# Kernel tuning notes

Hardware: AMD Instinct MI355X
Metric: run time of the kernel (lower is better)

Reference implementation:

```python
import jax, jax.numpy as jnp
import numpy as np
from jax import lax

B, CIN, H, W = 64, 3, 64, 64
HID = 128          # hidden_dim == embedding_dim
K = 1024           # num_embeddings
BETA = 0.25        # commitment cost


def _conv(x, w, b, stride):
    # torch Conv2d, padding=0, NCHW / OIHW weights
    y = lax.conv_general_dilated(x, w, (stride, stride), 'VALID',
                                 dimension_numbers=('NCHW', 'OIHW', 'NCHW'))
    return y + b[None, :, None, None]


def _conv_transpose(x, w, b, stride):
    # torch ConvTranspose2d, padding=0; w is [Cin, Cout, kh, kw] (torch layout)
    kh, kw = w.shape[2], w.shape[3]
    w2 = jnp.flip(w, (2, 3)).transpose(1, 0, 2, 3)  # -> OIHW, spatially flipped
    y = lax.conv_general_dilated(x, w2, (1, 1),
                                 [(kh - 1, kh - 1), (kw - 1, kw - 1)],
                                 lhs_dilation=(stride, stride),
                                 dimension_numbers=('NCHW', 'OIHW', 'NCHW'))
    return y + b[None, :, None, None]


def setup_inputs() -> dict:
    key = jax.random.key(0)
    ks = jax.random.split(key, 10)
    s = 0.05
    return {
        'x':      jax.random.normal(ks[0], (B, CIN, H, W), jnp.float32),
        'enc_w1': jax.random.normal(ks[1], (HID, CIN, 4, 4), jnp.float32) * s,
        'enc_b1': jnp.zeros((HID,), jnp.float32),
        'enc_w2': jax.random.normal(ks[2], (HID, HID, 2, 2), jnp.float32) * s,
        'enc_b2': jnp.zeros((HID,), jnp.float32),
        'codebook': jax.random.uniform(ks[3], (K, HID), jnp.float32,
                                       minval=-1.0 / K, maxval=1.0 / K),
        'dec_w1': jax.random.normal(ks[4], (HID, HID, 2, 2), jnp.float32) * s,
        'dec_b1': jnp.zeros((HID,), jnp.float32),
        'dec_w2': jax.random.normal(ks[5], (HID, CIN, 4, 4), jnp.float32) * s,
        'dec_b2': jnp.zeros((CIN,), jnp.float32),
    }


def reference(x, enc_w1, enc_b1, enc_w2, enc_b2, codebook,
              dec_w1, dec_b1, dec_w2, dec_b2):
    # ---- encoder ----
    z = jax.nn.relu(_conv(x, enc_w1, enc_b1, 2))
    z = jax.nn.relu(_conv(z, enc_w2, enc_b2, 1))   # [B, HID, 30, 30]

    # ---- vector quantizer (faithful to torch reshape semantics) ----
    D = HID
    flat = z.reshape(-1, D)                        # [N, D], C-order rows
    # squared euclidean distances (argmin identical to torch.cdist argmin)
    d2 = (jnp.sum(flat * flat, axis=1, keepdims=True)
          - 2.0 * flat @ codebook.T
          + jnp.sum(codebook * codebook, axis=1)[None, :])  # [N, K]
    idx = jnp.argmin(d2, axis=1)                   # [N]
    quantized = codebook[idx].reshape(z.shape)

    e_latent = jnp.mean((lax.stop_gradient(quantized) - z) ** 2)
    q_latent = jnp.mean((quantized - lax.stop_gradient(z)) ** 2)
    loss = q_latent + BETA * e_latent

    q_st = z + lax.stop_gradient(quantized - z)    # straight-through

    n = flat.shape[0]
    avg_probs = jnp.zeros((K,), z.dtype).at[idx].add(1.0) / n
    perplexity = jnp.exp(-jnp.sum(avg_probs * jnp.log(avg_probs + 1e-10)))

    # ---- decoder ----
    y = jax.nn.relu(_conv_transpose(q_st, dec_w1, dec_b1, 1))
    x_recon = _conv_transpose(y, dec_w2, dec_b2, 2)  # [B, 3, 64, 64]
    return x_recon, loss, perplexity
```

## Files before the change

kernel.cpp:

```cpp
#include <hip/hip_runtime.h>

#define B_    64
#define CIN_  3
#define HW_   64
#define HID_  128
#define K_    1024
#define H1_   31
#define H2_   30
#define NROWS_ 57600
#define NELEM_ 7372800

typedef __bf16 bf16_t;
typedef __attribute__((ext_vector_type(8))) __bf16 bf16x8;
typedef __attribute__((ext_vector_type(4))) float f32x4;
typedef __attribute__((ext_vector_type(16))) float f32x16;

__global__ __launch_bounds__(256) void wprep_k(const float* __restrict__ ew1,
    const float* __restrict__ ew2, const float* __restrict__ dw1,
    const float* __restrict__ dw2, const float* __restrict__ cb,
    bf16_t* __restrict__ wc1, bf16_t* __restrict__ wc2,
    bf16_t* __restrict__ wd1, bf16_t* __restrict__ wt2,
    bf16_t* __restrict__ cbb, float* __restrict__ cnorm,
    unsigned* __restrict__ hist, float* __restrict__ sse) {
  int id = blockIdx.x * 256 + threadIdx.x;
  int t = id >> 14, co = (id >> 7) & 127, ci = id & 127;
  wc2[id] = (bf16_t)ew2[(co * 128 + ci) * 4 + t];
  wd1[id] = (bf16_t)dw1[(ci * 128 + co) * 4 + (3 - t)];
  if (id < 8192) {
    int n = id >> 9, k = id & 511;
    int tap = k >> 7, c = k & 127;
    if (n < 12) {
      int nco = n >> 2, ph = (n >> 1) & 1, pw = n & 1;
      int off = (tap >> 1) * 8 + (tap & 1) * 2;
      wt2[id] = (bf16_t)dw2[c * 48 + nco * 16 + ph * 4 + pw + off];
    } else {
      wt2[id] = (bf16_t)0.f;
    }
    int c1 = id >> 6, k1 = id & 63;
    wc1[id] = (bf16_t)(k1 < 48 ? ew1[c1 * 48 + k1] : 0.f);
  }
  if (id < K_) {
    float s0 = 0.f;
    for (int d = 0; d < HID_; d += 4) {
      float4 v = *(const float4*)&cb[id * HID_ + d];
      bf16_t tt[4] = {(bf16_t)v.x, (bf16_t)v.y, (bf16_t)v.z, (bf16_t)v.w};
      *(ushort4*)&((ushort*)cbb)[id * HID_ + d] = *(ushort4*)tt;
      float f0 = (float)tt[0], f1 = (float)tt[1];
      float f2 = (float)tt[2], f3 = (float)tt[3];
      s0 += f0 * f0 + f1 * f1 + f2 * f2 + f3 * f3;
    }
    cnorm[id] = s0;
    hist[id] = 0u;
  }
  if (id == 0) *sse = 0.f;
}

__global__ __launch_bounds__(256, 2) void conv1m_k(const float* __restrict__ x,
    const bf16_t* __restrict__ wc1, const float* __restrict__ bias,
    ushort* __restrict__ z1t) {
  __shared__ __align__(16) bf16_t as_[64 * 72];
  __shared__ __align__(16) bf16_t bs_[128 * 72];
  int b = blockIdx.x >> 4, rt = blockIdx.x & 15;
  int tid = threadIdx.x, wv = tid >> 6, ln = tid & 63;
  const float* xb = x + (size_t)b * 12288;
  #pragma unroll
  for (int it = 0; it < 16; ++it) {
    int e = it * 256 + tid;
    int p = e >> 6, k = e & 63;
    float v = 0.f;
    if (k < 48) {
      int ci = k >> 4, kh = (k >> 2) & 3, kw = k & 3;
      int row = 2 * rt + (p >> 5); if (row > 30) row = 30;
      int col = p & 31;            if (col > 30) col = 30;
      v = xb[ci * 4096 + (2 * row + kh) * 64 + 2 * col + kw];
    }
    as_[p * 72 + k] = (bf16_t)v;
  }
  {
    const float4* wg = (const float4*)wc1;
    #pragma unroll
    for (int it = 0; it < 4; ++it) {
      int fi = it * 256 + tid;
      int co = fi >> 3, k8 = fi & 7;
      *(float4*)&bs_[co * 72 + k8 * 8] = wg[fi];
    }
  }
  __syncthreads();
  int q = ln >> 4, l = ln & 15;
  f32x4 acc8[8];
  #pragma unroll
  for (int c = 0; c < 8; ++c) acc8[c] = (f32x4){0.f, 0.f, 0.f, 0.f};
  bf16x8 af[2];
  #pragma unroll
  for (int kk = 0; kk < 2; ++kk)
    af[kk] = *(const bf16x8*)&as_[(wv * 16 + l) * 72 + kk * 32 + q * 8];
  #pragma unroll
  for (int cot = 0; cot < 8; ++cot) {
    #pragma unroll
    for (int kk = 0; kk < 2; ++kk) {
      bf16x8 bf = *(const bf16x8*)&bs_[(cot * 16 + l) * 72 + kk * 32 + q * 8];
      acc8[cot] = __builtin_amdgcn_mfma_f32_16x16x32_bf16(af[kk], bf,
                                                          acc8[cot], 0, 0, 0);
    }
  }
  #pragma unroll
  for (int cot = 0; cot < 8; ++cot) {
    int co = cot * 16 + l;
    float bv = bias[co];
    #pragma unroll
    for (int r = 0; r < 4; ++r) {
      int pos = wv * 16 + q * 4 + r;
      int prow = 2 * rt + (pos >> 5), pcol = pos & 31;
      if (prow < 31 && pcol < 31) {
        float v = fmaxf(acc8[cot][r] + bv, 0.f);
        bf16_t h = (bf16_t)v;
        z1t[((size_t)(b * 1024 + prow * 32 + pcol)) * 128 + co] = *(ushort*)&h;
      }
    }
  }
}

__global__ __launch_bounds__(256, 2) void conv2m_k(const bf16_t* __restrict__ z1t,
    const bf16_t* __restrict__ wc2, const float* __restrict__ bias,
    ushort* __restrict__ zbuf) {
  __shared__ __align__(16) bf16_t as_[98 * 136];
  __shared__ __align__(16) bf16_t bs_[128 * 136];
  int blk = blockIdx.x;
  int b = blk / 15, rt = blk % 15;
  int tid = threadIdx.x, wv = tid >> 6, ln = tid & 63;
  const float4* src = (const float4*)(z1t + ((size_t)b * 1024 + rt * 64) * 128);
  #pragma unroll
  for (int s = 0; s < 7; ++s) {
    int f = s * 256 + tid;
    if (f < 1568) {
      int lp = f >> 4, c16 = f & 15;
      *(float4*)&as_[lp * 136 + c16 * 8] = src[f];
    }
  }
  int m = wv * 16 + (ln & 15), q = ln >> 4;
  f32x4 acc8[8];
  #pragma unroll
  for (int c = 0; c < 8; ++c) acc8[c] = (f32x4){0.f, 0.f, 0.f, 0.f};
  const float4* w4 = (const float4*)wc2;
  #pragma unroll
  for (int t = 0; t < 4; ++t) {
    __syncthreads();
    #pragma unroll
    for (int s = 0; s < 8; ++s) {
      int f = s * 256 + tid;
      int co = f >> 4, c16 = f & 15;
      *(float4*)&bs_[co * 136 + c16 * 8] = w4[t * 2048 + f];
    }
    __syncthreads();
    int off = (t >> 1) * 32 + (t & 1);
    bf16x8 af[4];
    #pragma unroll
    for (int kk = 0; kk < 4; ++kk)
      af[kk] = *(const bf16x8*)&as_[(m + off) * 136 + kk * 32 + q * 8];
    #pragma unroll
    for (int cot = 0; cot < 8; ++cot) {
      #pragma unroll
      for (int kk = 0; kk < 4; ++kk) {
        bf16x8 bf = *(const bf16x8*)&bs_[(cot * 16 + (ln & 15)) * 136 +
                                         kk * 32 + q * 8];
        acc8[cot] = __builtin_amdgcn_mfma_f32_16x16x32_bf16(af[kk], bf,
                                                            acc8[cot], 0, 0, 0);
      }
    }
  }
  #pragma unroll
  for (int cot = 0; cot < 8; ++cot) {
    int co = cot * 16 + (ln & 15);
    float bv = bias[co];
    #pragma unroll
    for (int r = 0; r < 4; ++r) {
      int mo = wv * 16 + q * 4 + r;
      int ocol = mo & 31;
      if (ocol < 30) {
        int orow = rt * 2 + (mo >> 5);
        float v = fmaxf(acc8[cot][r] + bv, 0.f);
        bf16_t h = (bf16_t)v;
        zbuf[(size_t)(b * HID_ + co) * 900 + orow * 30 + ocol] = *(ushort*)&h;
      }
    }
  }
}

__global__ __launch_bounds__(256, 2) void vq1_k(const bf16_t* __restrict__ zb,
    const bf16_t* __restrict__ cbb, const float* __restrict__ cnorm,
    int* __restrict__ idxArr, unsigned* __restrict__ hist,
    float* __restrict__ sse) {
  __shared__ float cns[K_];
  __shared__ float redS[128];
  __shared__ int   redI[128];
  int n0 = blockIdx.x * 128;
  int tid = threadIdx.x;
  int wv = tid >> 6, ln = tid & 63;
  int lr = ln & 31, lh = ln >> 5;
  {
    float4 cv = ((const float4*)cnorm)[tid];
    cv.x *= -0.5f; cv.y *= -0.5f; cv.z *= -0.5f; cv.w *= -0.5f;
    ((float4*)cns)[tid] = cv;
  }
  const ushort* za = (const ushort*)zb +
                     ((size_t)(n0 + wv * 32 + lr)) * 128 + lh * 8;
  bf16x8 af[8];
  #pragma unroll
  for (int ks = 0; ks < 8; ++ks) af[ks] = *(const bf16x8*)(za + ks * 16);
  const ushort* cbB = (const ushort*)cbb + (size_t)lr * 128 + lh * 8;
  bf16x8 bf0[8], bf1[8];
  #pragma unroll
  for (int ks = 0; ks < 8; ++ks) bf0[ks] = *(const bf16x8*)(cbB + ks * 16);
  float bS[16];
  int   bI[16];
  #pragma unroll
  for (int r = 0; r < 16; ++r) { bS[r] = -3.4e38f; bI[r] = 0; }
  __syncthreads();
  for (int nt = 0; nt < 32; nt += 2) {
    {
      const ushort* cbn = cbB + (size_t)(nt + 1) * 4096;
      #pragma unroll
      for (int ks = 0; ks < 8; ++ks)
        bf1[ks] = *(const bf16x8*)(cbn + ks * 16);
    }
    {
      float hv = cns[nt * 32 + lr];
      f32x16 acc;
      #pragma unroll
      for (int r = 0; r < 16; ++r) acc[r] = hv;
      #pragma unroll
      for (int ks = 0; ks < 8; ++ks)
        acc = __builtin_amdgcn_mfma_f32_32x32x16_bf16(af[ks], bf0[ks], acc,
                                                      0, 0, 0);
      int code = nt * 32 + lr;
      #pragma unroll
      for (int r = 0; r < 16; ++r)
        if (acc[r] > bS[r]) { bS[r] = acc[r]; bI[r] = code; }
    }
    if (nt + 2 < 32) {
      const ushort* cbn = cbB + (size_t)(nt + 2) * 4096;
      #pragma unroll
      for (int ks = 0; ks < 8; ++ks)
        bf0[ks] = *(const bf16x8*)(cbn + ks * 16);
    }
    {
      float hv = cns[(nt + 1) * 32 + lr];
      f32x16 acc;
      #pragma unroll
      for (int r = 0; r < 16; ++r) acc[r] = hv;
      #pragma unroll
      for (int ks = 0; ks < 8; ++ks)
        acc = __builtin_amdgcn_mfma_f32_32x32x16_bf16(af[ks], bf1[ks], acc,
                                                      0, 0, 0);
      int code = (nt + 1) * 32 + lr;
      #pragma unroll
      for (int r = 0; r < 16; ++r)
        if (acc[r] > bS[r]) { bS[r] = acc[r]; bI[r] = code; }
    }
  }
  #pragma unroll
  for (int r = 0; r < 16; ++r) {
    float s = bS[r]; int i = bI[r];
    #pragma unroll
    for (int o = 16; o > 0; o >>= 1) {
      float os = __shfl_xor(s, o, 64); int oi = __shfl_xor(i, o, 64);
      if (os > s || (os == s && oi < i)) { s = os; i = oi; }
    }
    bS[r] = s; bI[r] = i;
  }
  if (lr == 0) {
    #pragma unroll
    for (int r = 0; r < 16; ++r) {
      int row = (r & 3) + 4 * lh + 8 * (r >> 2);
      redS[wv * 32 + row] = bS[r];
      redI[wv * 32 + row] = bI[r];
    }
  }
  __syncthreads();
  if (tid < 128) {
    int bi = redI[tid];
    float sbest = redS[tid];
    idxArr[n0 + tid] = bi;
    atomicAdd(&hist[bi], 1u);
    const ushort* zr = (const ushort*)zb + (size_t)(n0 + tid) * 128;
    float zn = 0.f;
    #pragma unroll
    for (int sg = 0; sg < 16; ++sg) {
      bf16x8 v = *(const bf16x8*)(zr + sg * 8);
      #pragma unroll
      for (int e = 0; e < 8; ++e) {
        float fv = (float)v[e];
        zn = fmaf(fv, fv, zn);
      }
    }
    float se = zn - 2.f * sbest;
    #pragma unroll
    for (int o = 32; o > 0; o >>= 1) se += __shfl_down(se, o, 64);
    if (ln == 0) atomicAdd(sse, se);
  }
}

__global__ __launch_bounds__(256) void tqz_k(const bf16_t* __restrict__ cbb,
    const int* __restrict__ idxArr, ushort* __restrict__ qt) {
  __shared__ ushort t[60 * 128];
  int bid = blockIdx.x, tid = threadIdx.x;
  if (bid < 960) {
    int b = bid / 15, st = bid % 15;
    int s0 = st * 60;
    #pragma unroll
    for (int it = 0; it < 8; ++it) {
      int task = it * 256 + tid;
      if (task < 1920) {
        int sc = task >> 7, c = task & 127;
        int f = b * 115200 + c * 900 + s0 + sc * 4;
        int n = f >> 7, d = f & 127;
        int k = idxArr[n];
        ushort4 v = *(const ushort4*)((const ushort*)cbb + k * 128 + d);
        t[(sc * 4 + 0) * 128 + c] = v.x;
        t[(sc * 4 + 1) * 128 + c] = v.y;
        t[(sc * 4 + 2) * 128 + c] = v.z;
        t[(sc * 4 + 3) * 128 + c] = v.w;
      }
    }
    __syncthreads();
    #pragma unroll
    for (int it = 0; it < 4; ++it) {
      int task = it * 256 + tid;
      if (task < 960) {
        int sl = task >> 4, c16 = task & 15;
        int s = s0 + sl;
        int h = s / 30, w = s - h * 30;
        int p = (h + 1) * 32 + (w + 1);
        *(uint4*)&qt[((size_t)(b * 1024 + p)) * 128 + c16 * 8] =
            *(uint4*)&t[sl * 128 + c16 * 8];
      }
    }
  } else {
    int zb_ = (bid - 960) * 4;
    uint4 zz = {0u, 0u, 0u, 0u};
    for (int e = tid; e < 4 * 124 * 16; e += 256) {
      int bb = zb_ + e / (124 * 16);
      int rem = e % (124 * 16);
      int pe = rem >> 4, s16 = rem & 15;
      int p;
      if (pe < 32) p = pe;
      else if (pe < 64) p = 31 * 32 + (pe - 32);
      else {
        int idx = pe - 64;
        p = (1 + (idx >> 1)) * 32 + ((idx & 1) ? 31 : 0);
      }
      *(uint4*)&qt[((size_t)(bb * 1024 + p)) * 128 + s16 * 8] = zz;
    }
  }
}

__global__ __launch_bounds__(256, 2) void convt1m_k(const bf16_t* __restrict__ qt,
    const bf16_t* __restrict__ wd1, const float* __restrict__ bias,
    ushort* __restrict__ yt) {
  __shared__ __align__(16) bf16_t as_[98 * 136];
  __shared__ __align__(16) bf16_t bs_[128 * 136];
  int blk = blockIdx.x;
  int b = blk >> 4, rt = blk & 15;
  int tid = threadIdx.x, wv = tid >> 6, ln = tid & 63;
  {
    uint4 zz = {0u, 0u, 0u, 0u};
    ushort* ytb = yt + (size_t)b * 1156 * 128;
    int nrows = (rt < 15) ? 2 : 1;
    int r0 = 2 * rt + 1;
    for (int e = tid; e < nrows * 48; e += 256) {
      int rr = e / 48, rem = e % 48, cc = rem / 16, s16 = rem % 16;
      int col = (cc == 0) ? 0 : (cc == 1 ? 32 : 33);
      *(uint4*)&ytb[((size_t)((r0 + rr) * 34 + col)) * 128 + s16 * 8] = zz;
    }
    if (rt == 0)
      for (int e = tid; e < 34 * 16; e += 256)
        *(uint4*)&ytb[((size_t)(e >> 4)) * 128 + (e & 15) * 8] = zz;
    if (rt == 15)
      for (int e = tid; e < 2 * 34 * 16; e += 256) {
        int rr = 32 + e / 544, rem = e % 544;
        *(uint4*)&ytb[((size_t)(rr * 34 + (rem >> 4))) * 128 + (rem & 15) * 8]
            = zz;
      }
  }
  const float4* src = (const float4*)(qt + (size_t)b * 1024 * 128);
  #pragma unroll
  for (int s = 0; s < 7; ++s) {
    int f = s * 256 + tid;
    if (f < 1568) {
      int lp = f >> 4, c16 = f & 15;
      int gr = rt * 64 + lp;
      if (gr > 1023) gr = 1023;
      *(float4*)&as_[lp * 136 + c16 * 8] = src[gr * 16 + c16];
    }
  }
  int m = wv * 16 + (ln & 15), q = ln >> 4;
  f32x4 acc8[8];
  #pragma unroll
  for (int c = 0; c < 8; ++c) acc8[c] = (f32x4){0.f, 0.f, 0.f, 0.f};
  const float4* w4 = (const float4*)wd1;
  #pragma unroll
  for (int t = 0; t < 4; ++t) {
    __syncthreads();
    #pragma unroll
    for (int s = 0; s < 8; ++s) {
      int f = s * 256 + tid;
      int co = f >> 4, c16 = f & 15;
      *(float4*)&bs_[co * 136 + c16 * 8] = w4[t * 2048 + f];
    }
    __syncthreads();
    int off = (t >> 1) * 32 + (t & 1);
    bf16x8 af[4];
    #pragma unroll
    for (int kk = 0; kk < 4; ++kk)
      af[kk] = *(const bf16x8*)&as_[(m + off) * 136 + kk * 32 + q * 8];
    #pragma unroll
    for (int cot = 0; cot < 8; ++cot) {
      #pragma unroll
      for (int kk = 0; kk < 4; ++kk) {
        bf16x8 bf = *(const bf16x8*)&bs_[(cot * 16 + (ln & 15)) * 136 +
                                         kk * 32 + q * 8];
        acc8[cot] = __builtin_amdgcn_mfma_f32_16x16x32_bf16(af[kk], bf,
                                                            acc8[cot], 0, 0, 0);
      }
    }
  }
  #pragma unroll
  for (int cot = 0; cot < 8; ++cot) {
    int co = cot * 16 + (ln & 15);
    float bv = bias[co];
    #pragma unroll
    for (int r = 0; r < 4; ++r) {
      int mo = wv * 16 + q * 4 + r;
      int orow = rt * 2 + (mo >> 5), ocol = mo & 31;
      if (orow < 31 && ocol < 31) {
        float v = fmaxf(acc8[cot][r] + bv, 0.f);
        bf16_t h = (bf16_t)v;
        yt[((size_t)b * 1156 + (orow + 1) * 34 + (ocol + 1)) * 128 + co] =
            *(ushort*)&h;
      }
    }
  }
}

__global__ __launch_bounds__(256, 2) void convt2m_k(const bf16_t* __restrict__ yt,
    const bf16_t* __restrict__ wt2, const float* __restrict__ bias,
    const unsigned* __restrict__ hist, const float* __restrict__ sse,
    float* __restrict__ out) {
  __shared__ __align__(16) bf16_t as_[128 * 136];
  __shared__ float redf[256];
  int b = blockIdx.x >> 4, rt = blockIdx.x & 15;
  int tid = threadIdx.x, wv = tid >> 6, ln = tid & 63;
  const float4* src = (const float4*)(yt + ((size_t)b * 1156 + rt * 68) * 128);
  #pragma unroll
  for (int s = 0; s < 8; ++s) {
    int f = s * 256 + tid;
    int lp = f >> 4, c16 = f & 15;
    *(float4*)&as_[lp * 136 + c16 * 8] = src[f];
  }
  __syncthreads();
  int mloc = wv * 16 + (ln & 15), q = ln >> 4;
  int qh = mloc >> 5, qw = mloc & 31;
  int base = (qh + 1) * 34 + qw + 1;
  f32x4 acc = {0.f, 0.f, 0.f, 0.f};
  #pragma unroll
  for (int kc = 0; kc < 16; ++kc) {
    int tap = kc >> 2;
    int toff = (tap & 1) + (tap >> 1) * 34;
    bf16x8 af = *(const bf16x8*)&as_[(base - toff) * 136 +
                                     (kc & 3) * 32 + q * 8];
    bf16x8 bf = *(const bf16x8*)&wt2[(size_t)(ln & 15) * 512 + kc * 32 + q * 8];
    acc = __builtin_amdgcn_mfma_f32_16x16x32_bf16(af, bf, acc, 0, 0, 0);
  }
  __syncthreads();
  float* bb = (float*)as_;
  #pragma unroll
  for (int r = 0; r < 4; ++r)
    bb[(wv * 16 + q * 4 + r) * 16 + (ln & 15)] = acc[r];
  __syncthreads();
  if (tid < 192) {
    int row_id = tid >> 4;
    int co = row_id >> 2, ohoff = row_id & 3;
    int qhl = ohoff >> 1, ph = ohoff & 1;
    float bv = bias[co];
    int ow0 = (tid & 15) * 4;
    float tmp[4];
    #pragma unroll
    for (int e = 0; e < 4; ++e) {
      int ow = ow0 + e;
      tmp[e] = bb[(qhl * 32 + (ow >> 1)) * 16 + co * 4 + ph * 2 + (ow & 1)]
               + bv;
    }
    *(float4*)&out[((size_t)(b * 3 + co)) * 4096 + (rt * 4 + ohoff) * 64 + ow0]
        = *(float4*)tmp;
  }
  if (blockIdx.x == 0) {
    float e = 0.f;
    for (int k = tid; k < K_; k += 256) {
      float p = (float)hist[k] * (1.0f / (float)NROWS_);
      e += p * logf(p + 1e-10f);
    }
    redf[tid] = e;
    __syncthreads();
    #pragma unroll
    for (int t = 128; t > 0; t >>= 1) {
      if (tid < t) redf[tid] += redf[tid + t];
      __syncthreads();
    }
    if (tid == 0) {
      out[786432] = 1.25f * (*sse) * (1.0f / (float)NELEM_);
      out[786433] = expf(-redf[0]);
    }
  }
}

extern "C" void kernel_launch(void* const* d_in, const int* in_sizes, int n_in,
                              void* d_out, int out_size, void* d_ws,
                              size_t ws_size, hipStream_t stream) {
  (void)in_sizes; (void)n_in; (void)out_size; (void)ws_size;
  const float* x   = (const float*)d_in[0];
  const float* ew1 = (const float*)d_in[1];
  const float* eb1 = (const float*)d_in[2];
  const float* ew2 = (const float*)d_in[3];
  const float* eb2 = (const float*)d_in[4];
  const float* cb  = (const float*)d_in[5];
  const float* dw1 = (const float*)d_in[6];
  const float* db1 = (const float*)d_in[7];
  const float* dw2 = (const float*)d_in[8];
  const float* db2 = (const float*)d_in[9];
  float* out = (float*)d_out;
  char* ws = (char*)d_ws;

  ushort*   yt    = (ushort*)(ws);
  bf16_t*   z1t   = (bf16_t*)(ws + 65175552);
  bf16_t*   qt    = (bf16_t*)(ws + 65175552);
  ushort*   zbuf  = (ushort*)(ws + 81985536);
  bf16_t*   cbb   = (bf16_t*)(ws + 96731136);
  bf16_t*   wc2   = (bf16_t*)(ws + 96993280);
  bf16_t*   wd1   = (bf16_t*)(ws + 97124352);
  int*      idxArr= (int*)(ws + 97255424);
  unsigned* hist  = (unsigned*)(ws + 97485824);
  float*    cnorm = (float*)(ws + 97489920);
  float*    sse   = (float*)(ws + 97494016);
  bf16_t*   wt2   = (bf16_t*)(ws + 97497088);
  bf16_t*   wc1   = (bf16_t*)(ws + 97513472);

  wprep_k<<<dim3(256), dim3(256), 0, stream>>>(ew1, ew2, dw1, dw2, cb,
                                               wc1, wc2, wd1, wt2,
                                               cbb, cnorm, hist, sse);
  conv1m_k<<<dim3(1024), dim3(256), 0, stream>>>(x, wc1, eb1, (ushort*)z1t);
  conv2m_k<<<dim3(960), dim3(256), 0, stream>>>(z1t, wc2, eb2, zbuf);
  vq1_k<<<dim3(450), dim3(256), 0, stream>>>((const bf16_t*)zbuf, cbb, cnorm,
                                             idxArr, hist, sse);
  tqz_k<<<dim3(976), dim3(256), 0, stream>>>(cbb, idxArr, (ushort*)qt);
  convt1m_k<<<dim3(1024), dim3(256), 0, stream>>>(qt, wd1, db1, yt);
  convt2m_k<<<dim3(1024), dim3(256), 0, stream>>>((const bf16_t*)yt, wt2, db2,
                                                  hist, sse, out);
}
```

Before: 259.8 us.

## Stage codebook chunks in LDS with double buffering and split VQ block over codes

The VQ argmin kernel now has each block cooperatively load 64-code codebook chunks into padded, double-buffered shared memory, so waves no longer each stream the whole codebook from global memory into registers. Each block handles 64 rows instead of 128, and its four waves form a 2x2 split over rows and code halves. A final cross-wave step merges the two partial argmins per row. The grid doubles to 900 blocks and the occupancy hint rises to 4, at the cost of extra barriers and shared-memory traffic.

Result: no change. 260.0 us (+0.1%).

```diff
diff --git a/kernel.cpp b/kernel.cpp
--- a/kernel.cpp
+++ b/kernel.cpp
@@ -186,77 +186,106 @@
   }
 }
 
-__global__ __launch_bounds__(256, 2) void vq1_k(const bf16_t* __restrict__ zb,
+__global__ __launch_bounds__(256, 4) void vq1_k(const bf16_t* __restrict__ zb,
     const bf16_t* __restrict__ cbb, const float* __restrict__ cnorm,
     int* __restrict__ idxArr, unsigned* __restrict__ hist,
     float* __restrict__ sse) {
+  __shared__ __align__(16) bf16_t cbs0[64 * 136];
+  __shared__ __align__(16) bf16_t cbs1[64 * 136];
   __shared__ float cns[K_];
-  __shared__ float redS[128];
-  __shared__ int   redI[128];
-  int n0 = blockIdx.x * 128;
+  __shared__ float redS[2][64];
+  __shared__ int   redI[2][64];
+  int n0 = blockIdx.x * 64;
   int tid = threadIdx.x;
   int wv = tid >> 6, ln = tid & 63;
   int lr = ln & 31, lh = ln >> 5;
+  int mt = wv & 1, pt = wv >> 1;
   {
     float4 cv = ((const float4*)cnorm)[tid];
     cv.x *= -0.5f; cv.y *= -0.5f; cv.z *= -0.5f; cv.w *= -0.5f;
     ((float4*)cns)[tid] = cv;
   }
   const ushort* za = (const ushort*)zb +
-                     ((size_t)(n0 + wv * 32 + lr)) * 128 + lh * 8;
+                     ((size_t)(n0 + mt * 32 + lr)) * 128 + lh * 8;
   bf16x8 af[8];
   #pragma unroll
   for (int ks = 0; ks < 8; ++ks) af[ks] = *(const bf16x8*)(za + ks * 16);
-  const ushort* cbB = (const ushort*)cbb + (size_t)lr * 128 + lh * 8;
-  bf16x8 bf0[8], bf1[8];
-  #pragma unroll
-  for (int ks = 0; ks < 8; ++ks) bf0[ks] = *(const bf16x8*)(cbB + ks * 16);
+  const float4* cg4 = (const float4*)cbb;
+  float4 pf[4];
+  #pragma unroll
+  for (int s = 0; s < 4; ++s) pf[s] = cg4[s * 256 + tid];
+  #pragma unroll
+  for (int s = 0; s < 4; ++s) {
+    int f = s * 256 + tid;
+    *(float4*)&cbs0[(f >> 4) * 136 + (f & 15) * 8] = pf[s];
+  }
+  #pragma unroll
+  for (int s = 0; s < 4; ++s)
+    pf[s] = cg4[1024 + s * 256 + tid];
   float bS[16];
   int   bI[16];
   #pragma unroll
   for (int r = 0; r < 16; ++r) { bS[r] = -3.4e38f; bI[r] = 0; }
+  int arow = (pt * 32 + lr) * 136 + lh * 8;
   __syncthreads();
-  for (int nt = 0; nt < 32; nt += 2) {
+  #pragma unroll 1
+  for (int c = 0; c < 16; c += 2) {
+    #pragma unroll
+    for (int s = 0; s < 4; ++s) {
+      int f = s * 256 + tid;
+      *(float4*)&cbs1[(f >> 4) * 136 + (f & 15) * 8] = pf[s];
+    }
+    if (c + 2 < 16) {
+      #pragma unroll
+      for (int s = 0; s < 4; ++s)
+        pf[s] = cg4[(c + 2) * 1024 + s * 256 + tid];
+    }
     {
-      const ushort* cbn = cbB + (size_t)(nt + 1) * 4096;
-      #pragma unroll
-      for (int ks = 0; ks < 8; ++ks)
-        bf1[ks] = *(const bf16x8*)(cbn + ks * 16);
-    }
-    {
-      float hv = cns[nt * 32 + lr];
+      int code = c * 64 + pt * 32 + lr;
+      float hv = cns[code];
       f32x16 acc;
       #pragma unroll
       for (int r = 0; r < 16; ++r) acc[r] = hv;
       #pragma unroll
-      for (int ks = 0; ks < 8; ++ks)
-        acc = __builtin_amdgcn_mfma_f32_32x32x16_bf16(af[ks], bf0[ks], acc,
+      for (int ks = 0; ks < 8; ++ks) {
+        bf16x8 bfr = *(const bf16x8*)&cbs0[arow + ks * 16];
+        acc = __builtin_amdgcn_mfma_f32_32x32x16_bf16(af[ks], bfr, acc,
                                                       0, 0, 0);
-      int code = nt * 32 + lr;
+      }
       #pragma unroll
       for (int r = 0; r < 16; ++r)
         if (acc[r] > bS[r]) { bS[r] = acc[r]; bI[r] = code; }
     }
-    if (nt + 2 < 32) {
-      const ushort* cbn = cbB + (size_t)(nt + 2) * 4096;
-      #pragma unroll
-      for (int ks = 0; ks < 8; ++ks)
-        bf0[ks] = *(const bf16x8*)(cbn + ks * 16);
+    __syncthreads();
+    if (c + 2 < 16) {
+      #pragma unroll
+      for (int s = 0; s < 4; ++s) {
+        int f = s * 256 + tid;
+        *(float4*)&cbs0[(f >> 4) * 136 + (f & 15) * 8] = pf[s];
+      }
+    }
+    if (c + 3 < 16) {
+      #pragma unroll
+      for (int s = 0; s < 4; ++s)
+        pf[s] = cg4[(c + 3) * 1024 + s * 256 + tid];
     }
     {
-      float hv = cns[(nt + 1) * 32 + lr];
+      int code = (c + 1) * 64 + pt * 32 + lr;
+      float hv = cns[code];
       f32x16 acc;
       #pragma unroll
       for (int r = 0; r < 16; ++r) acc[r] = hv;
       #pragma unroll
-      for (int ks = 0; ks < 8; ++ks)
-        acc = __builtin_amdgcn_mfma_f32_32x32x16_bf16(af[ks], bf1[ks], acc,
+      for (int ks = 0; ks < 8; ++ks) {
+        bf16x8 bfr = *(const bf16x8*)&cbs1[arow + ks * 16];
+        acc = __builtin_amdgcn_mfma_f32_32x32x16_bf16(af[ks], bfr, acc,
                                                       0, 0, 0);
-      int code = (nt + 1) * 32 + lr;
+      }
       #pragma unroll
       for (int r = 0; r < 16; ++r)
         if (acc[r] > bS[r]) { bS[r] = acc[r]; bI[r] = code; }
     }
+    __syncthreads();
   }
   #pragma unroll
   for (int r = 0; r < 16; ++r) {
@@ -271,15 +300,18 @@
   if (lr == 0) {
     #pragma unroll
     for (int r = 0; r < 16; ++r) {
-      int row = (r & 3) + 4 * lh + 8 * (r >> 2);
-      redS[wv * 32 + row] = bS[r];
-      redI[wv * 32 + row] = bI[r];
+      int row = (r & 3) + 8 * (r >> 2) + 4 * lh;
+      redS[pt][mt * 32 + row] = bS[r];
+      redI[pt][mt * 32 + row] = bI[r];
     }
   }
   __syncthreads();
-  if (tid < 128) {
-    int bi = redI[tid];
-    float sbest = redS[tid];
+  if (tid < 64) {
+    float s0 = redS[0][tid], s1 = redS[1][tid];
+    int i0 = redI[0][tid], i1 = redI[1][tid];
+    bool t = (s1 > s0) || (s1 == s0 && i1 < i0);
+    float sbest = t ? s1 : s0;
+    int bi = t ? i1 : i0;
     idxArr[n0 + tid] = bi;
     atomicAdd(&hist[bi], 1u);
     const ushort* zr = (const ushort*)zb + (size_t)(n0 + tid) * 128;
@@ -296,7 +328,7 @@
     float se = zn - 2.f * sbest;
     #pragma unroll
     for (int o = 32; o > 0; o >>= 1) se += __shfl_down(se, o, 64);
-    if (ln == 0) atomicAdd(sse, se);
+    if (tid == 0) atomicAdd(sse, se);
   }
 }
 
@@ -549,7 +581,7 @@
                                                cbb, cnorm, hist, sse);
   conv1m_k<<<dim3(1024), dim3(256), 0, stream>>>(x, wc1, eb1, (ushort*)z1t);
   conv2m_k<<<dim3(960), dim3(256), 0, stream>>>(z1t, wc2, eb2, zbuf);
-  vq1_k<<<dim3(450), dim3(256), 0, stream>>>((const bf16_t*)zbuf, cbb, cnorm,
+  vq1_k<<<dim3(900), dim3(256), 0, stream>>>((const bf16_t*)zbuf, cbb, cnorm,
                                              idxArr, hist, sse);
   tqz_k<<<dim3(976), dim3(256), 0, stream>>>(cbb, idxArr, (ushort*)qt);
   convt1m_k<<<dim3(1024), dim3(256), 0, stream>>>(qt, wd1, db1, yt);
```
